# Optimization experiments

Measured on AMD Instinct MI355X. Metric: run time of the kernel, lower is better.

## Reference

```python
import jax, jax.numpy as jnp
import numpy as np

K = 16          # k_neighbours
BIG = 1e9       # distance penalty for masked senders


def setup_inputs() -> dict:
    key = jax.random.key(0)
    ks = jax.random.split(key, 8)
    B, N, F, H, FO = 64, 512, 64, 128, 64
    nodes = jax.random.normal(ks[0], (B, N, F), jnp.float32)
    mask = jax.random.randint(ks[1], (B, N), 0, 2, jnp.int32)

    def w(k_, sh):
        return jax.random.normal(k_, sh, jnp.float32) * (1.0 / np.sqrt(sh[0]).astype(np.float32))

    We1 = w(ks[2], (2 * F, H)); be1 = jnp.zeros((H,), jnp.float32)
    We2 = w(ks[3], (H, H));     be2 = jnp.zeros((H,), jnp.float32)
    Wn1 = w(ks[4], (F + H, H)); bn1 = jnp.zeros((H,), jnp.float32)
    Wn2 = w(ks[5], (H, FO));    bn2 = jnp.zeros((FO,), jnp.float32)
    return dict(nodes=nodes, mask=mask, We1=We1, be1=be1, We2=We2, be2=be2,
                Wn1=Wn1, bn1=bn1, Wn2=Wn2, bn2=bn2)


def reference(nodes, mask, We1, be1, We2, be2, Wn1, bn1, Wn2, bn2):
    # nodes: [B,N,F] ; mask: [B,N] (1 = real node, 0 = padding)
    m = mask.astype(nodes.dtype)                      # [B,N]
    x = nodes * m[..., None]                          # zero padded nodes

    # --- dynamic kNN graph (euclidean_squared + top_k, no self connection) ---
    sq = jnp.sum(x * x, axis=-1)                      # [B,N]
    dist = jnp.abs(sq[:, :, None] + sq[:, None, :]
                   - 2.0 * jnp.einsum('bnf,bmf->bnm', x, x))  # [B,N,N]
    dist = dist + BIG * (1.0 - m)[:, None, :]         # never select masked senders
    _, idx = jax.lax.top_k(-dist, K + 1)              # [B,N,K+1]
    idx = idx[..., 1:]                                # drop self connection -> [B,N,K]

    # --- gather sender features / masks along edges ---
    gathered = jax.vmap(lambda xf, ib: xf[ib])(x, idx)    # [B,N,K,F]
    smask = jax.vmap(lambda mv, ib: mv[ib])(m, idx)       # [B,N,K]
    recv = jnp.broadcast_to(x[:, :, None, :], gathered.shape)
    edges = jnp.concatenate([recv, gathered], axis=-1)    # [B,N,K,2F] ('concat' aggregation)

    # --- edge MLP (gather-compute) ---
    h = jax.nn.relu(edges @ We1 + be1)
    h = jax.nn.relu(h @ We2 + be2)                        # [B,N,K,H]

    # --- masked mean pooling over edges (scatter back to nodes) ---
    emask = m[:, :, None] * smask                         # edge valid iff both endpoints valid
    h = h * emask[..., None]
    cnt = jnp.maximum(jnp.sum(emask, axis=-1, keepdims=True), 1.0)  # [B,N,1]
    pooled = jnp.sum(h, axis=2) / cnt                     # [B,N,H]

    # --- node update MLP ---
    nh = jnp.concatenate([x, pooled], axis=-1)            # [B,N,F+H]
    out = jax.nn.relu(nh @ Wn1 + bn1) @ Wn2 + bn2         # [B,N,FO]
    return out * m[..., None]                             # zero padded nodes in output
```

## Files before the change

### kernel.cpp

```cpp
#include <hip/hip_runtime.h>

#define DI __device__ __forceinline__

typedef __bf16 bf16_t;
typedef __bf16 bf16x4 __attribute__((ext_vector_type(4)));
typedef __bf16 bf16x8 __attribute__((ext_vector_type(8)));
typedef float f32x4 __attribute__((ext_vector_type(4)));
typedef unsigned long long u64;


DI bf16_t f2b(float f) {
  unsigned u = __float_as_uint(f);
  unsigned r = (u + 0x7fffu + ((u >> 16) & 1u)) >> 16;
  return __builtin_bit_cast(bf16_t, (unsigned short)r);
}
DI float b2f(bf16_t h) {
  return __uint_as_float(((unsigned)__builtin_bit_cast(unsigned short, h)) << 16);
}
DI f32x4 zero4() { f32x4 z = {0.f, 0.f, 0.f, 0.f}; return z; }

DI bf16x8 make_frag(const float* p, bool wantlo) {
  float4 v0 = *(const float4*)p;
  float4 v1 = *(const float4*)(p + 4);
  float vv[8] = {v0.x, v0.y, v0.z, v0.w, v1.x, v1.y, v1.z, v1.w};
  bf16x8 a;
#pragma unroll
  for (int j = 0; j < 8; ++j) {
    bf16_t hi = f2b(vv[j]);
    a[j] = wantlo ? f2b(vv[j] - b2f(hi)) : hi;
  }
  return a;
}
DI void make_frag2(const float* p, bf16x8* hi, bf16x8* lo) {
  float4 v0 = *(const float4*)p;
  float4 v1 = *(const float4*)(p + 4);
  float vv[8] = {v0.x, v0.y, v0.z, v0.w, v1.x, v1.y, v1.z, v1.w};
#pragma unroll
  for (int j = 0; j < 8; ++j) {
    bf16_t h = f2b(vv[j]);
    (*hi)[j] = h;
    (*lo)[j] = f2b(vv[j] - b2f(h));
  }
}

DI u64 u64min(u64 a, u64 b) { return a < b ? a : b; }
template <int CTRL>
DI u64 dpp_u64(u64 v) {
  int lo = (int)(unsigned)(v & 0xffffffffull);
  int hi = (int)(unsigned)(v >> 32);
  int tlo = __builtin_amdgcn_update_dpp(0, lo, CTRL, 0xF, 0xF, true);
  int thi = __builtin_amdgcn_update_dpp(0, hi, CTRL, 0xF, 0xF, true);
  return (((u64)(unsigned)thi) << 32) | (unsigned)tlo;
}
template <int CTRL>
DI float dpp_f32(float v) {
  int t = __builtin_amdgcn_update_dpp(0, (int)__float_as_uint(v), CTRL, 0xF, 0xF, true);
  return __uint_as_float((unsigned)t);
}
DI u64 rowmin_u64(u64 v) {
  v = u64min(v, dpp_u64<0xB1>(v));
  v = u64min(v, dpp_u64<0x4E>(v));
  v = u64min(v, dpp_u64<0x141>(v));
  v = u64min(v, dpp_u64<0x140>(v));
  return v;
}
DI float rowsum_f32(float v) {
  v += dpp_f32<0xB1>(v);
  v += dpp_f32<0x4E>(v);
  v += dpp_f32<0x141>(v);
  v += dpp_f32<0x140>(v);
  return v;
}
DI void bitonic16(u64* a) {
#pragma unroll
  for (int k = 2; k <= 16; k <<= 1)
#pragma unroll
    for (int j = k >> 1; j > 0; j >>= 1)
#pragma unroll
      for (int i = 0; i < 16; ++i) {
        const int l = i ^ j;
        if (l > i) {
          const bool up = ((i & k) == 0);
          const bool sw = up ? (a[i] > a[l]) : (a[i] < a[l]);
          const u64 t0 = a[i], t1 = a[l];
          a[i] = sw ? t1 : t0;
          a[l] = sw ? t0 : t1;
        }
      }
}
DI void sorted_insert16(u64* a, u64 k) {
  u64 na[16];
#pragma unroll
  for (int p = 0; p < 16; ++p) {
    const bool cur_gt = (a[p] > k);
    const bool prv_le = (p == 0) ? true : (a[p - 1] <= k);
    na[p] = !cur_gt ? a[p] : (prv_le ? k : a[p - 1]);
  }
#pragma unroll
  for (int p = 0; p < 16; ++p) a[p] = na[p];
}

__global__ void __launch_bounds__(256) kfuse(const float* __restrict__ nodes,
    const int* __restrict__ mask,
    const float* __restrict__ We1, const float* __restrict__ We2,
    const float* __restrict__ Wn1, const float* __restrict__ Wn2,
    float* __restrict__ x, bf16_t* __restrict__ xhi, bf16_t* __restrict__ xlo,
    float* __restrict__ sq, int* __restrict__ vlist, int* __restrict__ vcnt,
    bf16_t* __restrict__ W1p, bf16_t* __restrict__ W2p,
    bf16_t* __restrict__ Wn1p, bf16_t* __restrict__ Wn2p) {
  const int blk = blockIdx.x, t = threadIdx.x;
  __shared__ int cnts[8];
  __shared__ int basep[8];

  if (blk < 512) {
    const int b = blk >> 3, n0 = (blk & 7) * 64;
#pragma unroll
    for (int i = 0; i < 4; ++i) {
      const int idx = t + 256 * i;
      const int gi = b * 512 + n0 + (idx >> 4);
      const int fo = (idx & 15) * 4;
      const float fm = (float)mask[gi];
      const size_t ro = (size_t)gi * 64;
      float4 v = *(const float4*)(nodes + ro + fo);
      v.x *= fm; v.y *= fm; v.z *= fm; v.w *= fm;
      *(float4*)(x + ro + fo) = v;
      float vv[4] = {v.x, v.y, v.z, v.w};
      bf16x4 hh, ll;
#pragma unroll
      for (int k = 0; k < 4; ++k) {
        bf16_t hi = f2b(vv[k]);
        hh[k] = hi;
        ll[k] = f2b(vv[k] - b2f(hi));
      }
      *(bf16x4*)(xhi + ro + fo) = hh;
      *(bf16x4*)(xlo + ro + fo) = ll;
      float s = v.x * v.x + v.y * v.y + v.z * v.z + v.w * v.w;
      s = rowsum_f32(s);
      if ((t & 15) == 0) sq[gi] = s;
    }
  } else if (blk < 576) {
    const int b = blk - 512, lane = t & 63, w = t >> 6;
    unsigned long long bal[2]; int flag[2];
#pragma unroll
    for (int h = 0; h < 2; ++h) {
      flag[h] = (mask[b * 512 + h * 256 + t] != 0);
      bal[h] = __ballot(flag[h]);
      if (lane == 0) cnts[h * 4 + w] = __popcll(bal[h]);
    }
    __syncthreads();
    if (t == 0) {
      int a = 0;
      for (int c = 0; c < 8; ++c) { basep[c] = a; a += cnts[c]; }
      vcnt[b] = a;
    }
    __syncthreads();
#pragma unroll
    for (int h = 0; h < 2; ++h) {
      if (flag[h]) {
        const unsigned long long lt = (lane == 0) ? 0ull : (~0ull >> (64 - lane));
        const int pos = basep[h * 4 + w] + __popcll(bal[h] & lt);
        vlist[b * 512 + pos] = h * 256 + t;
      }
    }
  } else {
    int p = (blk - 576) * 256 + t;
    const float* W; bf16_t* dst; int K, Nn, local, mode;
    if (p < 4096)       { W = We1; dst = W1p;  K = 128; Nn = 128; mode = 0; local = p; }
    else if (p < 8192)  { W = We2; dst = W2p;  K = 128; Nn = 128; mode = 1; local = p - 4096; }
    else if (p < 14336) { W = Wn1; dst = Wn1p; K = 192; Nn = 128; mode = 0; local = p - 8192; }
    else                { W = Wn2; dst = Wn2p; K = 128; Nn = 64;  mode = 1; local = p - 14336; }
    int lane = local & 63;
    int nnt = (Nn >> 4);
    int chunk = local >> 6;
    int nt = chunk % nnt;
    int s = chunk / nnt;
    int n = nt * 16 + (lane & 15);
    int kbase = s * 32 + ((lane >> 4) * 8);
    bf16x8 v;
#pragma unroll
    for (int j = 0; j < 8; ++j) {
      int kp = kbase + j;
      int region = kp / K;
      int kk = kp - region * K;
      float w = W[kk * Nn + n];
      bf16_t hi = f2b(w);
      v[j] = (mode == 1 && region == 1) ? f2b(w - b2f(hi)) : hi;
    }
    *(bf16x8*)(dst + (size_t)local * 8) = v;
  }
}

__global__ void __launch_bounds__(256) kknn(const bf16_t* __restrict__ xhi,
    const bf16_t* __restrict__ xlo,
    const float* __restrict__ sq, const int* __restrict__ vlist,
    const int* __restrict__ vcnt, int* __restrict__ idxg) {
  const int b = blockIdx.x & 63, tile = blockIdx.x >> 6;
  const int nv = vcnt[b];
  if (tile * 16 >= nv) return;
  const int t = threadIdx.x, lane = t & 63, w = t >> 6;
  const int i = lane >> 4, d = lane & 15;
  __shared__ float sqs[512];
  __shared__ int vls[512];
  __shared__ __align__(16) float S[16 * 520];
  for (int k = t; k < 512; k += 256) { sqs[k] = sq[b * 512 + k]; vls[k] = vlist[b * 512 + k]; }
  __syncthreads();

  const size_t xb = (size_t)b * 512 * 64;

  const int aslot = tile * 16 + d;
  const int arow = vls[aslot < nv ? aslot : 0];
  bf16x8 ah[2], al[2];
#pragma unroll
  for (int kh = 0; kh < 2; ++kh) {
    ah[kh] = *(const bf16x8*)(xhi + xb + (size_t)arow * 64 + kh * 32 + i * 8);
    al[kh] = *(const bf16x8*)(xlo + xb + (size_t)arow * 64 + kh * 32 + i * 8);
  }

  const int rslot = tile * 16 + w * 4 + i;
  const bool vrow = (rslot < nv);
  const int nrow = vls[rslot < nv ? rslot : 0];
  const float sqn = sqs[nrow];

  int crs[8];
#pragma unroll
  for (int jj = 0; jj < 8; ++jj) {
    const int c = (w + 4 * jj) * 16 + d;
    crs[jj] = vls[c < nv ? c : 0];
  }

  bf16x8 pbh[4][2], pbl[4][2];
#pragma unroll
  for (int jj = 0; jj < 4; ++jj) {
    if ((w + 4 * jj) * 16 < nv) {
#pragma unroll
      for (int kh = 0; kh < 2; ++kh) {
        pbh[jj][kh] = *(const bf16x8*)(xhi + xb + (size_t)crs[jj] * 64 + kh * 32 + i * 8);
        pbl[jj][kh] = *(const bf16x8*)(xlo + xb + (size_t)crs[jj] * 64 + kh * 32 + i * 8);
      }
    }
  }
#pragma unroll
  for (int jj = 0; jj < 8; ++jj) {
    const int ct = w + 4 * jj;
    if (ct * 16 < nv) {
      const int sl = jj & 3;
      bf16x8 bh[2] = {pbh[sl][0], pbh[sl][1]};
      bf16x8 bl[2] = {pbl[sl][0], pbl[sl][1]};
      if (jj < 4 && (w + 4 * (jj + 4)) * 16 < nv) {
#pragma unroll
        for (int kh = 0; kh < 2; ++kh) {
          pbh[sl][kh] = *(const bf16x8*)(xhi + xb + (size_t)crs[jj + 4] * 64 + kh * 32 + i * 8);
          pbl[sl][kh] = *(const bf16x8*)(xlo + xb + (size_t)crs[jj + 4] * 64 + kh * 32 + i * 8);
        }
      }
      f32x4 acc = zero4();
#pragma unroll
      for (int kh = 0; kh < 2; ++kh) {
        acc = __builtin_amdgcn_mfma_f32_16x16x32_bf16(ah[kh], bh[kh], acc, 0, 0, 0);
        acc = __builtin_amdgcn_mfma_f32_16x16x32_bf16(ah[kh], bl[kh], acc, 0, 0, 0);
        acc = __builtin_amdgcn_mfma_f32_16x16x32_bf16(al[kh], bh[kh], acc, 0, 0, 0);
        acc = __builtin_amdgcn_mfma_f32_16x16x32_bf16(al[kh], bl[kh], acc, 0, 0, 0);
      }
#pragma unroll
      for (int r = 0; r < 4; ++r) S[(i * 4 + r) * 520 + ct * 16 + d] = acc[r];
    }
  }
  __syncthreads();

  const u64 INF64 = ~0ull;
  u64 s1[16];
#pragma unroll
  for (int j = 0; j < 16; ++j) s1[j] = INF64;
#pragma unroll
  for (int j = 0; j < 16; ++j) {
    if (j * 16 < nv) {
      const int c = j * 16 + d;
      const int m = vls[c < nv ? c : 0];
      const float dot = S[(w * 4 + i) * 520 + j * 16 + d];
      const float dd = fabsf(sqn + sqs[m] - 2.f * dot);
      const u64 key = (((u64)__float_as_uint(dd)) << 32) | (unsigned)m;
      const bool ok = (c < nv) && (m != nrow);
      s1[j] = ok ? key : INF64;
    }
  }
  bitonic16(s1);
  for (int j = 16; j * 16 < nv; ++j) {
    const int c = j * 16 + d;
    const int m = vls[c < nv ? c : 0];
    const float dot = S[(w * 4 + i) * 520 + j * 16 + d];
    const float dd = fabsf(sqn + sqs[m] - 2.f * dot);
    const u64 key = (((u64)__float_as_uint(dd)) << 32) | (unsigned)m;
    const bool ok = (c < nv) && (m != nrow);
    sorted_insert16(s1, ok ? key : INF64);
  }

  int res = nrow;
#pragma unroll
  for (int ts = 0; ts < 16; ++ts) {
    const u64 wmin = rowmin_u64(s1[0]);
    if (d == ts) res = (wmin == INF64) ? nrow : (int)(unsigned)(wmin & 0xffffffffull);
    const bool w1 = (wmin != INF64) && (s1[0] == wmin);
#pragma unroll
    for (int k = 0; k < 15; ++k) s1[k] = w1 ? s1[k + 1] : s1[k];
    s1[15] = w1 ? INF64 : s1[15];
  }
  if (vrow) idxg[((size_t)b * 512 + rslot) * 16 + d] = res;
}

__global__ void __launch_bounds__(256, 2) kedge(const bf16_t* __restrict__ xhi,
    const bf16_t* __restrict__ xlo, const int* __restrict__ idxg,
    const int* __restrict__ vlist, const int* __restrict__ vcnt,
    const bf16_t* __restrict__ W1p, const bf16_t* __restrict__ W2p,
    const float* __restrict__ be1, const float* __restrict__ be2,
    float* __restrict__ pooled) {
  __shared__ __align__(16) bf16_t wbuf[16384];
  __shared__ __align__(16) bf16_t hfrag[4][2][512];
  const int t = threadIdx.x, lane = t & 63, w = t >> 6;
  const int q = lane >> 4, e = lane & 15;
  const int bb = blockIdx.x & 63;
  const int s0 = ((blockIdx.x >> 6) * 4 + w) * 2;

  {
    const uint4* s1 = (const uint4*)W1p;
    uint4* dst = (uint4*)wbuf;
#pragma unroll
    for (int i = 0; i < 8; ++i) dst[t + 256 * i] = s1[t + 256 * i];
  }
  __syncthreads();

  const int nv = vcnt[bb];
  if (s0 >= nv) return;

  int vl[2], sv[2];
#pragma unroll
  for (int u = 0; u < 2; ++u) {
    const int sl = (s0 + u) < nv ? (s0 + u) : 0;
    vl[u] = vlist[bb * 512 + sl];
    sv[u] = idxg[((size_t)(bb * 512 + sl) << 4) + e];
  }

  for (int base = s0; base < nv; base += 64) {
    const bool act1 = (base + 1) < nv;
    const int gid0 = bb * 512 + vl[0];
    const int gid1 = bb * 512 + vl[1];
    const size_t rb0 = (size_t)gid0 << 6;
    const size_t rb1 = (size_t)gid1 << 6;
    const size_t nb0 = (size_t)(bb * 512 + sv[0]) << 6;
    const size_t nb1 = (size_t)(bb * 512 + sv[1]) << 6;

    bf16x8 af[2][8];
#pragma unroll
    for (int k = 0; k < 4; ++k) {
      const int off = (k & 1) * 32 + q * 8;
      const bf16_t* pl = (k >> 1) ? xlo : xhi;
      af[0][k]     = *(const bf16x8*)(pl + rb0 + off);
      af[1][k]     = *(const bf16x8*)(pl + rb1 + off);
      af[0][4 + k] = *(const bf16x8*)(pl + nb0 + off);
      af[1][4 + k] = *(const bf16x8*)(pl + nb1 + off);
    }

    int nvl[2] = {vl[0], vl[1]}, nsv[2] = {sv[0], sv[1]};
    {
      const int nb = base + 64;
      if (nb < nv) {
#pragma unroll
        for (int u = 0; u < 2; ++u) {
          const int sl = (nb + u) < nv ? (nb + u) : 0;
          nvl[u] = vlist[bb * 512 + sl];
          nsv[u] = idxg[((size_t)(bb * 512 + sl) << 4) + e];
        }
      }
    }

    f32x4 acc[2][8];
#pragma unroll
    for (int u = 0; u < 2; ++u)
#pragma unroll
      for (int nt = 0; nt < 8; ++nt) acc[u][nt] = zero4();

#pragma unroll
    for (int ph = 0; ph < 2; ++ph)
#pragma unroll
      for (int inner = 0; inner < 2; ++inner) {
        const bf16_t* wb = wbuf + (ph * 2 + inner) * 4096;
        const bf16x8 h0 = af[0][ph * 4 + inner];
        const bf16x8 h1 = af[1][ph * 4 + inner];
        const bf16x8 l0 = af[0][ph * 4 + 2 + inner];
        const bf16x8 l1 = af[1][ph * 4 + 2 + inner];
#pragma unroll
        for (int nt = 0; nt < 8; ++nt) {
          const bf16x8 bfv = *(const bf16x8*)(wb + (nt * 64 + lane) * 8);
          acc[0][nt] = __builtin_amdgcn_mfma_f32_16x16x32_bf16(h0, bfv, acc[0][nt], 0, 0, 0);
          acc[0][nt] = __builtin_amdgcn_mfma_f32_16x16x32_bf16(l0, bfv, acc[0][nt], 0, 0, 0);
          acc[1][nt] = __builtin_amdgcn_mfma_f32_16x16x32_bf16(h1, bfv, acc[1][nt], 0, 0, 0);
          acc[1][nt] = __builtin_amdgcn_mfma_f32_16x16x32_bf16(l1, bfv, acc[1][nt], 0, 0, 0);
        }
      }

    f32x4 acc2[2][8];
#pragma unroll
    for (int u = 0; u < 2; ++u)
#pragma unroll
      for (int nt = 0; nt < 8; ++nt) acc2[u][nt] = zero4();

#pragma unroll
    for (int qq = 0; qq < 4; ++qq) {
#pragma unroll
      for (int u = 0; u < 2; ++u)
#pragma unroll
        for (int nt2 = 0; nt2 < 2; ++nt2) {
          const int nt = qq * 2 + nt2;
          const int cc = nt * 16 + e;
          const float bv = be1[cc];
          const int bse = (q * 4 + 16 * ((cc >> 3) & 3)) * 8 + (cc & 7);
#pragma unroll
          for (int r = 0; r < 4; ++r)
            hfrag[w][u][bse + r * 8] = f2b(fmaxf(acc[u][nt][r] + bv, 0.f));
        }
      {
        const bf16x8 a20 = *(const bf16x8*)(&hfrag[w][0][lane * 8]);
        const bf16x8 a21 = *(const bf16x8*)(&hfrag[w][1][lane * 8]);
        const bf16_t* wb2 = W2p + qq * 4096;
#pragma unroll
        for (int nt = 0; nt < 8; ++nt) {
          const bf16x8 bfv = *(const bf16x8*)(wb2 + (nt * 64 + lane) * 8);
          acc2[0][nt] = __builtin_amdgcn_mfma_f32_16x16x32_bf16(a20, bfv, acc2[0][nt], 0, 0, 0);
          acc2[1][nt] = __builtin_amdgcn_mfma_f32_16x16x32_bf16(a21, bfv, acc2[1][nt], 0, 0, 0);
        }
      }
    }

#pragma unroll
    for (int u = 0; u < 2; ++u) {
      if (u == 0 || act1) {
        const int gid = u ? gid1 : gid0;
#pragma unroll
        for (int nt = 0; nt < 8; ++nt) {
          const float bv = be2[nt * 16 + e];
          float part = 0.f;
#pragma unroll
          for (int r = 0; r < 4; ++r) part += fmaxf(acc2[u][nt][r] + bv, 0.f);
          part += __shfl_xor(part, 16, 64);
          part += __shfl_xor(part, 32, 64);
          if (lane < 16) pooled[(size_t)gid * 128 + nt * 16 + lane] = part * 0.0625f;
        }
      }
    }

    vl[0] = nvl[0]; vl[1] = nvl[1];
    sv[0] = nsv[0]; sv[1] = nsv[1];
  }
}

__global__ void __launch_bounds__(256, 2) knode(const float* __restrict__ x,
    const float* __restrict__ pooled, const int* __restrict__ mask,
    const bf16_t* __restrict__ Wn1p, const bf16_t* __restrict__ Wn2p,
    const float* __restrict__ bn1, const float* __restrict__ bn2,
    float* __restrict__ out) {
  __shared__ __align__(16) bf16_t wbuf[32768];
  __shared__ __align__(16) bf16_t hfrag[4][1024];
  const int t = threadIdx.x, lane = t & 63, w = t >> 6;
  const int q = lane >> 4, e = lane & 15;
  const int nodebase = (blockIdx.x * 4 + w) * 16;

  {
    const uint4* s1 = (const uint4*)Wn1p;
    const uint4* s2 = (const uint4*)Wn2p;
    uint4* dst = (uint4*)wbuf;
#pragma unroll
    for (int i = 0; i < 12; ++i) dst[t + 256 * i] = s1[t + 256 * i];
#pragma unroll
    for (int i = 0; i < 4; ++i) dst[3072 + t + 256 * i] = s2[t + 256 * i];
  }
  __syncthreads();

  f32x4 acc[8];
#pragma unroll
  for (int nt = 0; nt < 8; ++nt) acc[nt] = zero4();

#pragma unroll
  for (int sr = 0; sr < 6; ++sr) {
    const int col = sr * 32 + q * 8;
    const int node = nodebase + e;
    const float* p = (col < 64) ? (x + (size_t)node * 64 + col)
                                : (pooled + (size_t)node * 128 + (col - 64));
    bf16x8 afh, afl;
    make_frag2(p, &afh, &afl);
#pragma unroll
    for (int nt = 0; nt < 8; ++nt) {
      const bf16x8 bfv = *(const bf16x8*)(wbuf + sr * 4096 + (nt * 64 + lane) * 8);
      acc[nt] = __builtin_amdgcn_mfma_f32_16x16x32_bf16(afh, bfv, acc[nt], 0, 0, 0);
      acc[nt] = __builtin_amdgcn_mfma_f32_16x16x32_bf16(afl, bfv, acc[nt], 0, 0, 0);
    }
  }

  f32x4 acc2[4];
#pragma unroll
  for (int nt = 0; nt < 4; ++nt) acc2[nt] = zero4();

#pragma unroll
  for (int hh = 0; hh < 2; ++hh) {
#pragma unroll
    for (int nt4 = 0; nt4 < 4; ++nt4) {
      const int nt = hh * 4 + nt4;
      const int cc = nt * 16 + e;
      const float bv = bn1[cc];
      const int bse = (((cc >> 5) & 1) * 64 + q * 4 + 16 * ((cc >> 3) & 3)) * 8 + (cc & 7);
#pragma unroll
      for (int r = 0; r < 4; ++r)
        hfrag[w][bse + r * 8] = f2b(fmaxf(acc[nt][r] + bv, 0.f));
    }
#pragma unroll
    for (int sl = 0; sl < 2; ++sl) {
      const int f = hh * 2 + sl;
      const bf16x8 a2 = *(const bf16x8*)(&hfrag[w][(sl * 64 + lane) * 8]);
      const bf16_t* wb2 = wbuf + 24576 + f * 2048;
#pragma unroll
      for (int nt = 0; nt < 4; ++nt) {
        const bf16x8 bfv = *(const bf16x8*)(wb2 + (nt * 64 + lane) * 8);
        acc2[nt] = __builtin_amdgcn_mfma_f32_16x16x32_bf16(a2, bfv, acc2[nt], 0, 0, 0);
      }
    }
  }

  int mm[4];
#pragma unroll
  for (int r = 0; r < 4; ++r) mm[r] = mask[nodebase + q * 4 + r];
#pragma unroll
  for (int nt = 0; nt < 4; ++nt) {
    const float bv = bn2[nt * 16 + e];
#pragma unroll
    for (int r = 0; r < 4; ++r) {
      const int node = nodebase + q * 4 + r;
      out[(size_t)node * 64 + nt * 16 + e] = (acc2[nt][r] + bv) * (float)mm[r];
    }
  }
}

extern "C" void kernel_launch(void* const* d_in, const int* in_sizes, int n_in,
                              void* d_out, int out_size, void* d_ws, size_t ws_size,
                              hipStream_t stream) {
  const float* nodes = (const float*)d_in[0];
  const int*   mask  = (const int*)d_in[1];
  const float* We1   = (const float*)d_in[2];
  const float* be1   = (const float*)d_in[3];
  const float* We2   = (const float*)d_in[4];
  const float* be2   = (const float*)d_in[5];
  const float* Wn1   = (const float*)d_in[6];
  const float* bn1   = (const float*)d_in[7];
  const float* Wn2   = (const float*)d_in[8];
  const float* bn2   = (const float*)d_in[9];
  float* out = (float*)d_out;

  char* p = (char*)d_ws;
  auto alloc = [&](size_t bytes) -> char* {
    char* r = p;
    p += (bytes + 255) & ~(size_t)255;
    return r;
  };
  float*  x      = (float*)alloc((size_t)32768 * 64 * 4);
  bf16_t* xhi    = (bf16_t*)alloc((size_t)32768 * 64 * 2);
  bf16_t* xlo    = (bf16_t*)alloc((size_t)32768 * 64 * 2);
  float*  sq     = (float*)alloc((size_t)32768 * 4);
  int*    vlist  = (int*)alloc((size_t)32768 * 4);
  int*    vcnt   = (int*)alloc((size_t)64 * 4);
  int*    idxg   = (int*)alloc((size_t)32768 * 16 * 4);
  float*  pooled = (float*)alloc((size_t)32768 * 128 * 4);
  bf16_t* W1p    = (bf16_t*)alloc((size_t)8 * 8 * 64 * 8 * 2);
  bf16_t* W2p    = (bf16_t*)alloc((size_t)8 * 8 * 64 * 8 * 2);
  bf16_t* Wn1p   = (bf16_t*)alloc((size_t)12 * 8 * 64 * 8 * 2);
  bf16_t* Wn2p   = (bf16_t*)alloc((size_t)8 * 4 * 64 * 8 * 2);
  if ((size_t)(p - (char*)d_ws) > ws_size) return;

  kfuse<<<640, 256, 0, stream>>>(nodes, mask, We1, We2, Wn1, Wn2,
                                 x, xhi, xlo, sq, vlist, vcnt, W1p, W2p, Wn1p, Wn2p);
  kknn<<<2048, 256, 0, stream>>>(xhi, xlo, sq, vlist, vcnt, idxg);
  kedge<<<512, 256, 0, stream>>>(xhi, xlo, idxg, vlist, vcnt, W1p, W2p, be1, be2, pooled);
  knode<<<512, 256, 0, stream>>>(x, pooled, mask, Wn1p, Wn2p, bn1, bn2, out);
}
```

Measured before the change: 176.3 us.

## Stage W2 in LDS and process one node per wave with 512-thread blocks

The edge kernel now uses 512-thread blocks (8 waves). Each wave handles one node per iteration instead of two. W2 is copied into shared memory alongside W1, so the second matmul reads its B fragments from LDS rather than global memory, and the first-layer activations are staged in LDS to fit this single-node layout. This cuts per-wave register pressure and removes the global W2 reads, but it doubles LDS per block and halves reuse of each weight fragment per load, which may limit occupancy.

```diff
diff --git a/kernel.cpp b/kernel.cpp
--- a/kernel.cpp
+++ b/kernel.cpp
@@ -307,148 +307,119 @@
   if (vrow) idxg[((size_t)b * 512 + rslot) * 16 + d] = res;
 }
 
-__global__ void __launch_bounds__(256, 2) kedge(const bf16_t* __restrict__ xhi,
+__global__ void __launch_bounds__(512, 2) kedge(const bf16_t* __restrict__ xhi,
     const bf16_t* __restrict__ xlo, const int* __restrict__ idxg,
     const int* __restrict__ vlist, const int* __restrict__ vcnt,
     const bf16_t* __restrict__ W1p, const bf16_t* __restrict__ W2p,
     const float* __restrict__ be1, const float* __restrict__ be2,
     float* __restrict__ pooled) {
-  __shared__ __align__(16) bf16_t wbuf[16384];
-  __shared__ __align__(16) bf16_t hfrag[4][2][512];
+  __shared__ __align__(16) bf16_t wbuf[32768];
+  __shared__ __align__(16) bf16_t hfrag[8][1024];
   const int t = threadIdx.x, lane = t & 63, w = t >> 6;
   const int q = lane >> 4, e = lane & 15;
   const int bb = blockIdx.x & 63;
-  const int s0 = ((blockIdx.x >> 6) * 4 + w) * 2;
+  const int s0 = (blockIdx.x >> 6) * 8 + w;
 
   {
     const uint4* s1 = (const uint4*)W1p;
+    const uint4* s2 = (const uint4*)W2p;
     uint4* dst = (uint4*)wbuf;
 #pragma unroll
-    for (int i = 0; i < 8; ++i) dst[t + 256 * i] = s1[t + 256 * i];
+    for (int i = 0; i < 4; ++i) dst[t + 512 * i] = s1[t + 512 * i];
+#pragma unroll
+    for (int i = 0; i < 4; ++i) dst[2048 + t + 512 * i] = s2[t + 512 * i];
   }
   __syncthreads();
 
   const int nv = vcnt[bb];
   if (s0 >= nv) return;
 
-  int vl[2], sv[2];
-#pragma unroll
-  for (int u = 0; u < 2; ++u) {
-    const int sl = (s0 + u) < nv ? (s0 + u) : 0;
-    vl[u] = vlist[bb * 512 + sl];
-    sv[u] = idxg[((size_t)(bb * 512 + sl) << 4) + e];
-  }
+  int vl = vlist[bb * 512 + s0];
+  int sv = idxg[((size_t)(bb * 512 + s0) << 4) + e];
 
   for (int base = s0; base < nv; base += 64) {
-    const bool act1 = (base + 1) < nv;
-    const int gid0 = bb * 512 + vl[0];
-    const int gid1 = bb * 512 + vl[1];
-    const size_t rb0 = (size_t)gid0 << 6;
-    const size_t rb1 = (size_t)gid1 << 6;
-    const size_t nb0 = (size_t)(bb * 512 + sv[0]) << 6;
-    const size_t nb1 = (size_t)(bb * 512 + sv[1]) << 6;
-
-    bf16x8 af[2][8];
+    const int gid = bb * 512 + vl;
+    const size_t rb = (size_t)gid << 6;
+    const size_t nb = (size_t)(bb * 512 + sv) << 6;
+
+    bf16x8 af[8];
 #pragma unroll
     for (int k = 0; k < 4; ++k) {
       const int off = (k & 1) * 32 + q * 8;
       const bf16_t* pl = (k >> 1) ? xlo : xhi;
-      af[0][k]     = *(const bf16x8*)(pl + rb0 + off);
-      af[1][k]     = *(const bf16x8*)(pl + rb1 + off);
-      af[0][4 + k] = *(const bf16x8*)(pl + nb0 + off);
-      af[1][4 + k] = *(const bf16x8*)(pl + nb1 + off);
-    }
-
-    int nvl[2] = {vl[0], vl[1]}, nsv[2] = {sv[0], sv[1]};
+      af[k]     = *(const bf16x8*)(pl + rb + off);
+      af[4 + k] = *(const bf16x8*)(pl + nb + off);
+    }
+
+    int nvl = vl, nsv = sv;
     {
-      const int nb = base + 64;
-      if (nb < nv) {
-#pragma unroll
-        for (int u = 0; u < 2; ++u) {
-          const int sl = (nb + u) < nv ? (nb + u) : 0;
-          nvl[u] = vlist[bb * 512 + sl];
-          nsv[u] = idxg[((size_t)(bb * 512 + sl) << 4) + e];
-        }
-      }
-    }
-
-    f32x4 acc[2][8];
-#pragma unroll
-    for (int u = 0; u < 2; ++u)
-#pragma unroll
-      for (int nt = 0; nt < 8; ++nt) acc[u][nt] = zero4();
+      const int nbs = base + 64;
+      if (nbs < nv) {
+        nvl = vlist[bb * 512 + nbs];
+        nsv = idxg[((size_t)(bb * 512 + nbs) << 4) + e];
+      }
+    }
+
+    f32x4 acc[8];
+#pragma unroll
+    for (int nt = 0; nt < 8; ++nt) acc[nt] = zero4();
 
 #pragma unroll
     for (int ph = 0; ph < 2; ++ph)
 #pragma unroll
       for (int inner = 0; inner < 2; ++inner) {
         const bf16_t* wb = wbuf + (ph * 2 + inner) * 4096;
-        const bf16x8 h0 = af[0][ph * 4 + inner];
-        const bf16x8 h1 = af[1][ph * 4 + inner];
-        const bf16x8 l0 = af[0][ph * 4 + 2 + inner];
-        const bf16x8 l1 = af[1][ph * 4 + 2 + inner];
+        const bf16x8 h = af[ph * 4 + inner];
+        const bf16x8 l = af[ph * 4 + 2 + inner];
 #pragma unroll
         for (int nt = 0; nt < 8; ++nt) {
           const bf16x8 bfv = *(const bf16x8*)(wb + (nt * 64 + lane) * 8);
-          acc[0][nt] = __builtin_amdgcn_mfma_f32_16x16x32_bf16(h0, bfv, acc[0][nt], 0, 0, 0);
-          acc[0][nt] = __builtin_amdgcn_mfma_f32_16x16x32_bf16(l0, bfv, acc[0][nt], 0, 0, 0);
-          acc[1][nt] = __builtin_amdgcn_mfma_f32_16x16x32_bf16(h1, bfv, acc[1][nt], 0, 0, 0);
-          acc[1][nt] = __builtin_amdgcn_mfma_f32_16x16x32_bf16(l1, bfv, acc[1][nt], 0, 0, 0);
+          acc[nt] = __builtin_amdgcn_mfma_f32_16x16x32_bf16(h, bfv, acc[nt], 0, 0, 0);
+          acc[nt] = __builtin_amdgcn_mfma_f32_16x16x32_bf16(l, bfv, acc[nt], 0, 0, 0);
         }
       }
 
-    f32x4 acc2[2][8];
-#pragma unroll
-    for (int u = 0; u < 2; ++u)
-#pragma unroll
-      for (int nt = 0; nt < 8; ++nt) acc2[u][nt] = zero4();
-
-#pragma unroll
-    for (int qq = 0; qq < 4; ++qq) {
-#pragma unroll
-      for (int u = 0; u < 2; ++u)
-#pragma unroll
-        for (int nt2 = 0; nt2 < 2; ++nt2) {
-          const int nt = qq * 2 + nt2;
-          const int cc = nt * 16 + e;
-          const float bv = be1[cc];
-          const int bse = (q * 4 + 16 * ((cc >> 3) & 3)) * 8 + (cc & 7);
-#pragma unroll
-          for (int r = 0; r < 4; ++r)
-            hfrag[w][u][bse + r * 8] = f2b(fmaxf(acc[u][nt][r] + bv, 0.f));
-        }
-      {
-        const bf16x8 a20 = *(const bf16x8*)(&hfrag[w][0][lane * 8]);
-        const bf16x8 a21 = *(const bf16x8*)(&hfrag[w][1][lane * 8]);
-        const bf16_t* wb2 = W2p + qq * 4096;
+    f32x4 acc2[8];
+#pragma unroll
+    for (int nt = 0; nt < 8; ++nt) acc2[nt] = zero4();
+
+#pragma unroll
+    for (int hh = 0; hh < 2; ++hh) {
+#pragma unroll
+      for (int nt4 = 0; nt4 < 4; ++nt4) {
+        const int nt = hh * 4 + nt4;
+        const int cc = nt * 16 + e;
+        const float bv = be1[cc];
+        const int bse = (((cc >> 5) & 1) * 64 + q * 4 + 16 * ((cc >> 3) & 3)) * 8 + (cc & 7);
+#pragma unroll
+        for (int r = 0; r < 4; ++r)
+          hfrag[w][bse + r * 8] = f2b(fmaxf(acc[nt][r] + bv, 0.f));
+      }
+#pragma unroll
+      for (int sl = 0; sl < 2; ++sl) {
+        const int f = hh * 2 + sl;
+        const bf16x8 a2 = *(const bf16x8*)(&hfrag[w][(sl * 64 + lane) * 8]);
+        const bf16_t* wb2 = wbuf + 16384 + f * 4096;
 #pragma unroll
         for (int nt = 0; nt < 8; ++nt) {
           const bf16x8 bfv = *(const bf16x8*)(wb2 + (nt * 64 + lane) * 8);
-          acc2[0][nt] = __builtin_amdgcn_mfma_f32_16x16x32_bf16(a20, bfv, acc2[0][nt], 0, 0, 0);
-          acc2[1][nt] = __builtin_amdgcn_mfma_f32_16x16x32_bf16(a21, bfv, acc2[1][nt], 0, 0, 0);
+          acc2[nt] = __builtin_amdgcn_mfma_f32_16x16x32_bf16(a2, bfv, acc2[nt], 0, 0, 0);
         }
       }
     }
 
 #pragma unroll
-    for (int u = 0; u < 2; ++u) {
-      if (u == 0 || act1) {
-        const int gid = u ? gid1 : gid0;
-#pragma unroll
-        for (int nt = 0; nt < 8; ++nt) {
-          const float bv = be2[nt * 16 + e];
-          float part = 0.f;
-#pragma unroll
-          for (int r = 0; r < 4; ++r) part += fmaxf(acc2[u][nt][r] + bv, 0.f);
-          part += __shfl_xor(part, 16, 64);
-          part += __shfl_xor(part, 32, 64);
-          if (lane < 16) pooled[(size_t)gid * 128 + nt * 16 + lane] = part * 0.0625f;
-        }
-      }
-    }
-
-    vl[0] = nvl[0]; vl[1] = nvl[1];
-    sv[0] = nsv[0]; sv[1] = nsv[1];
+    for (int nt = 0; nt < 8; ++nt) {
+      const float bv = be2[nt * 16 + e];
+      float part = 0.f;
+#pragma unroll
+      for (int r = 0; r < 4; ++r) part += fmaxf(acc2[nt][r] + bv, 0.f);
+      part += __shfl_xor(part, 16, 64);
+      part += __shfl_xor(part, 32, 64);
+      if (lane < 16) pooled[(size_t)gid * 128 + nt * 16 + lane] = part * 0.0625f;
+    }
+
+    vl = nvl; sv = nsv;
   }
 }
 
@@ -575,6 +546,6 @@
   kfuse<<<640, 256, 0, stream>>>(nodes, mask, We1, We2, Wn1, Wn2,
                                  x, xhi, xlo, sq, vlist, vcnt, W1p, W2p, Wn1p, Wn2p);
   kknn<<<2048, 256, 0, stream>>>(xhi, xlo, sq, vlist, vcnt, idxg);
-  kedge<<<512, 256, 0, stream>>>(xhi, xlo, idxg, vlist, vcnt, W1p, W2p, be1, be2, pooled);
+  kedge<<<512, 512, 0, stream>>>(xhi, xlo, idxg, vlist, vcnt, W1p, W2p, be1, be2, pooled);
   knode<<<512, 256, 0, stream>>>(x, pooled, mask, Wn1p, Wn2p, bn1, bn2, out);
 }
```

Result: faster. 167.7 us (-4.9%).
